# Kernel tuning notes

Measured on AMD Instinct MI355X. Metric: run time of the kernel, lower is better.

Reference implementation:

```python
import jax, jax.numpy as jnp
import numpy as np

B, N, D, K = 32, 2048, 512, 128
GAMMA = 10.0      # entropy_regularizer_weight
STEPS = 10        # optimization_steps
EPS = 1e-12


def _l2_normalize(x):
    return x * jax.lax.rsqrt(jnp.sum(x * x, axis=-1, keepdims=True) + EPS)


def setup_inputs() -> dict:
    key = jax.random.key(0)
    k1, k2, k3, k4 = jax.random.split(key, 4)
    features = jax.random.normal(k1, (B, N, D), dtype=jnp.float32)
    # transport ratio mu in (0,1): fraction of mass sent to the support
    transport_ratio = jax.random.uniform(k2, (B,), dtype=jnp.float32, minval=0.3, maxval=0.7)
    c_u = jax.random.uniform(k3, (B, N), dtype=jnp.float32)
    limit = float(np.sqrt(6.0 / (K + D)))  # GlorotUniform for (K, D) weight
    target_support = jax.random.uniform(k4, (K, D), dtype=jnp.float32, minval=-limit, maxval=limit)
    return {"features": features, "transport_ratio": transport_ratio,
            "c_u": c_u, "target_support": target_support}


def reference(features, transport_ratio, c_u, target_support):
    # --- binary costs: pairwise squared L2 between l2-normalized support and features ---
    f = _l2_normalize(features)          # [B, N, D]
    t = _l2_normalize(target_support)    # [K, D]
    cb = (jnp.sum(t * t, axis=-1)[None, :, None]
          + jnp.sum(f * f, axis=-1)[:, None, :]
          - 2.0 * jnp.einsum('kd,bnd->bkn', t, f))          # [B, K, N]
    C = jnp.concatenate([c_u[:, None, :], cb], axis=1)       # [B, K+1, N], row 0 = unary (discard) cost
    mu = transport_ratio[:, None, None]                      # [B, 1, 1]

    # --- entropy-regularized partial OT: Sinkhorn-style alternating scaling ---
    Q0 = jnp.exp(-GAMMA * C)
    n = jnp.asarray(C.shape[-1], C.dtype)

    def step(_, Q):
        # project onto column marginal: each feature carries mass 1/N
        Q = Q / (jnp.sum(Q, axis=1, keepdims=True) * n + EPS)
        # project onto row-mass constraints: support rows carry total mu, discard row 1-mu
        s0 = jnp.sum(Q[:, :1], axis=(1, 2), keepdims=True)
        ss = jnp.sum(Q[:, 1:], axis=(1, 2), keepdims=True)
        Q = jnp.concatenate([Q[:, :1] * (1.0 - mu) / (s0 + EPS),
                             Q[:, 1:] * mu / (ss + EPS)], axis=1)
        return Q

    Q = jax.lax.fori_loop(0, STEPS, step, Q0)
    # final column projection so each feature's transported mass is exactly 1/N
    P = Q / (jnp.sum(Q, axis=1, keepdims=True) * n + EPS)    # [B, K+1, N]
    return P
```

## Files before the change

### kernel.cpp

```cpp
#include <hip/hip_runtime.h>
#include <math.h>

#define B_ 32
#define N_ 2048
#define D_ 512
#define K_ 128
#define GAMMA_ 10.0f
#define EPS_ 1e-12f
#define STEPS_ 10
#define SHIFT_ 18.0f
#define EXP_NEG_SHIFT_ 1.5229979e-08f

typedef _Float16 f16x8 __attribute__((ext_vector_type(8)));
typedef _Float16 f16x4 __attribute__((ext_vector_type(4)));
typedef float f32x16 __attribute__((ext_vector_type(16)));

__global__ void k_prep_t(const float* __restrict__ ts, _Float16* __restrict__ tq,
                         float* __restrict__ rt, float* __restrict__ tnn) {
    int k = blockIdx.x;
    int lane = threadIdx.x;
    const float4* rp = (const float4*)(ts + (size_t)k * D_ + lane * 8);
    float4 v0 = rp[0], v1 = rp[1];
    f16x8 hv;
    hv[0] = (_Float16)v0.x; hv[1] = (_Float16)v0.y; hv[2] = (_Float16)v0.z; hv[3] = (_Float16)v0.w;
    hv[4] = (_Float16)v1.x; hv[5] = (_Float16)v1.y; hv[6] = (_Float16)v1.z; hv[7] = (_Float16)v1.w;
    float ssq = 0.f;
#pragma unroll
    for (int j = 0; j < 8; ++j) { float x = (float)hv[j]; ssq += x * x; }
#pragma unroll
    for (int off = 32; off; off >>= 1) ssq += __shfl_xor(ssq, off);
    if (lane == 0) {
        float rtv = (float)(1.0 / sqrt((double)ssq + 1e-12));
        rt[k] = rtv;
        tnn[k] = ssq * rtv * rtv;
    }
    *(f16x8*)&tq[((size_t)lane * 128 + k) * 8] = hv;
}

__global__ __launch_bounds__(256, 6) void k_gemm(
    const float* __restrict__ features,
    const _Float16* __restrict__ tq,
    const float* __restrict__ rt, const float* __restrict__ tnn,
    _Float16* __restrict__ E,
    float* __restrict__ A1)
{
    __shared__ _Float16 Bf[2][32 * 64];
    __shared__ float rowssq[32];
    __shared__ float csum[4][32];
    __shared__ float ldsrt[128], ldstnn[128];

    const int tid = threadIdx.x;
    const int b = blockIdx.x >> 6;
    const int n0 = (blockIdx.x & 63) * 32;
    const int w = tid >> 6;
    const int l = tid & 63;
    const int hi = l >> 5;
    const int l31 = l & 31;

    if (tid < 128) { ldsrt[tid] = rt[tid]; ldstnn[tid] = tnn[tid]; }

    const int fq = tid & 7;
    const int r0 = tid >> 3;
    const float4* fbase = (const float4*)(features + ((size_t)(b * N_ + n0)) * D_);

    float ss = 0.f;
    f32x16 acc;
#pragma unroll
    for (int i = 0; i < 16; ++i) acc[i] = 0.f;

    float4 br[2];
    f16x8 apre[4];

    auto stage_load = [&](int c) {
#pragma unroll
        for (int i = 0; i < 2; ++i)
            br[i] = fbase[(size_t)r0 * 128 + c * 16 + fq + i * 8];
    };

    auto a_load = [&](int c) {
#pragma unroll
        for (int ks = 0; ks < 4; ++ks) {
            int sB = ks * 2 + hi;
            size_t u = (size_t)(c * 8 + sB) * 128 + w * 32 + l31;
            apre[ks] = *(const f16x8*)&tq[u * 8];
        }
    };

    auto stage_write = [&](int buf) {
#pragma unroll
        for (int i = 0; i < 2; ++i) {
            float4 v = br[i];
            f16x4 hv;
            hv[0] = (_Float16)v.x; hv[1] = (_Float16)v.y;
            hv[2] = (_Float16)v.z; hv[3] = (_Float16)v.w;
            float q0 = (float)hv[0], q1 = (float)hv[1], q2 = (float)hv[2], q3 = (float)hv[3];
            ss += q0 * q0 + q1 * q1 + q2 * q2 + q3 * q3;
            int q = fq + i * 8;
            int s = q >> 1;
            int hh = q & 1;
            int idx = r0 * 64 + ((s ^ (r0 & 7)) << 3) + hh * 4;
            *(f16x4*)&Bf[buf][idx] = hv;
        }
    };

    auto compute = [&](int cur) {
#pragma unroll
        for (int ks = 0; ks < 4; ++ks) {
            int sB = ks * 2 + hi;
            f16x8 bfr = *(const f16x8*)&Bf[cur][l31 * 64 + ((sB ^ (l31 & 7)) << 3)];
            acc = __builtin_amdgcn_mfma_f32_32x32x16_f16(apre[ks], bfr, acc, 0, 0, 0);
        }
    };

    stage_load(0);
    a_load(0);
    stage_write(0);
    __syncthreads();

#pragma unroll
    for (int c = 0; c < 8; ++c) {
        int cur = c & 1;
        if (c < 7) stage_load(c + 1);
        compute(cur);
        if (c < 7) a_load(c + 1);
        if (c < 7) stage_write(cur ^ 1);
        __syncthreads();
    }

    ss += __shfl_xor(ss, 1);
    ss += __shfl_xor(ss, 2);
    ss += __shfl_xor(ss, 4);
    if (fq == 0) rowssq[r0] = ss;
    __syncthreads();

    const int n = n0 + l31;
    float rsq = rowssq[l31];
    float rf = (float)(1.0 / sqrt((double)rsq + 1e-12));
    float fnn = rsq * rf * rf;
    float cs = 0.f;
#pragma unroll
    for (int r = 0; r < 16; ++r) {
        int krow = (r & 3) + 8 * (r >> 2) + 4 * hi;
        int k = w * 32 + krow;
        float cb = ldstnn[k] + fnn - 2.0f * ldsrt[k] * rf * acc[r];
        float e = expf(SHIFT_ - GAMMA_ * cb);
        _Float16 eh = (_Float16)e;
        cs += (float)eh;
        E[((size_t)(b * K_ + k)) * N_ + n] = eh;
    }
    cs += __shfl_xor(cs, 32);
    if (!hi) csum[w][l31] = cs;
    __syncthreads();
    if (tid < 32)
        A1[b * N_ + n0 + tid] = csum[0][tid] + csum[1][tid] + csum[2][tid] + csum[3][tid];
}

__global__ __launch_bounds__(256) void k_sinkhorn(const float* __restrict__ tr,
                                                  const float* __restrict__ c_u,
                                                  const float* __restrict__ A1,
                                                  float* __restrict__ out,
                                                  float* __restrict__ wfb) {
    __shared__ float sc0[4], sc1[4], sres[2];
    int b = blockIdx.x, tid = threadIdx.x;
    float mu = tr[b];
    const float nf = (float)N_;
    float a0[8], a1[8], w[8];
#pragma unroll
    for (int r = 0; r < 8; ++r) {
        int n = tid + 256 * r;
        a0[r] = expf(-GAMMA_ * c_u[b * N_ + n]);
        a1[r] = A1[b * N_ + n] * EXP_NEG_SHIFT_;
        w[r] = 1.f;
    }
    float alpha = 1.f, beta = 1.f;
    for (int s = 0; s < STEPS_; ++s) {
        float p0 = 0.f, p1 = 0.f;
#pragma unroll
        for (int r = 0; r < 8; ++r) {
            float cs = w[r] * (alpha * a0[r] + beta * a1[r]);
            w[r] = w[r] / (cs * nf + EPS_);
            p0 += a0[r] * w[r];
            p1 += a1[r] * w[r];
        }
#pragma unroll
        for (int off = 32; off; off >>= 1) {
            p0 += __shfl_xor(p0, off);
            p1 += __shfl_xor(p1, off);
        }
        int wid = tid >> 6;
        if ((tid & 63) == 0) { sc0[wid] = p0; sc1[wid] = p1; }
        __syncthreads();
        if (tid == 0) {
            sres[0] = sc0[0] + sc0[1] + sc0[2] + sc0[3];
            sres[1] = sc1[0] + sc1[1] + sc1[2] + sc1[3];
        }
        __syncthreads();
        float s0 = alpha * sres[0], ssum = beta * sres[1];
        alpha *= (1.f - mu) / (s0 + EPS_);
        beta *= mu / (ssum + EPS_);
    }
#pragma unroll
    for (int r = 0; r < 8; ++r) {
        int n = tid + 256 * r;
        float cs = w[r] * (alpha * a0[r] + beta * a1[r]);
        float wf = w[r] / (cs * nf + EPS_);
        out[(size_t)b * (K_ + 1) * N_ + n] = alpha * a0[r] * wf;
        wfb[b * N_ + n] = beta * wf * EXP_NEG_SHIFT_;
    }
}

__global__ void k_scale(const _Float16* __restrict__ E, const float* __restrict__ wfb,
                        float* __restrict__ out) {
    size_t g = (size_t)blockIdx.x * 256 + threadIdx.x;
    size_t idx = g * 8;
    int b = (int)(idx >> 18);
    int rem = (int)(idx & ((K_ * N_) - 1));
    int k = rem >> 11, n = rem & (N_ - 1);
    f16x8 e = *(const f16x8*)&E[idx];
    float4 w0 = *(const float4*)&wfb[b * N_ + n];
    float4 w1 = *(const float4*)&wfb[b * N_ + n + 4];
    float* op = &out[((size_t)(b * (K_ + 1) + 1 + k)) * N_ + n];
    float4 o0, o1;
    o0.x = (float)e[0] * w0.x; o0.y = (float)e[1] * w0.y;
    o0.z = (float)e[2] * w0.z; o0.w = (float)e[3] * w0.w;
    o1.x = (float)e[4] * w1.x; o1.y = (float)e[5] * w1.y;
    o1.z = (float)e[6] * w1.z; o1.w = (float)e[7] * w1.w;
    *(float4*)op = o0;
    *(float4*)(op + 4) = o1;
}

extern "C" void kernel_launch(void* const* d_in, const int* in_sizes, int n_in,
                              void* d_out, int out_size, void* d_ws, size_t ws_size,
                              hipStream_t stream) {
    const float* features = (const float*)d_in[0];
    const float* tr = (const float*)d_in[1];
    const float* c_u = (const float*)d_in[2];
    const float* ts = (const float*)d_in[3];
    float* out = (float*)d_out;

    char* ws = (char*)d_ws;
    _Float16* tq = (_Float16*)ws;
    float* rt = (float*)(ws + 131072);
    float* tnn = (float*)(ws + 131584);
    float* A1 = (float*)(ws + 132096);
    float* wfb = (float*)(ws + 132096 + 262144);
    _Float16* E = (_Float16*)(ws + 132096 + 524288);
    (void)in_sizes; (void)n_in; (void)out_size; (void)ws_size;

    k_prep_t<<<K_, 64, 0, stream>>>(ts, tq, rt, tnn);
    k_gemm<<<B_ * 64, 256, 0, stream>>>(features, tq, rt, tnn, E, A1);
    k_sinkhorn<<<B_, 256, 0, stream>>>(tr, c_u, A1, out, wfb);
    k_scale<<<(B_ * K_ * N_) / (8 * 256), 256, 0, stream>>>(E, wfb, out);
}
```

Before: 54.63 us.

## Stage features into LDS via direct global-to-LDS loads as fp32

Features are now copied straight from global memory into an fp32 LDS double buffer with the async global_load_lds instruction, instead of going through registers, converting to fp16 and then storing. The fp16 conversion and the sum-of-squares row norm move into the MFMA compute loop, so each wave works out the row norms itself and the LDS reduction plus its extra barrier are gone. The aim is to cut register staging, VGPR pressure and store instructions. In exchange LDS use doubles, more conversion work sits on the critical compute path, and the norm is now computed from fp32 values rather than the fp16-rounded ones.

```diff
diff --git a/kernel.cpp b/kernel.cpp
--- a/kernel.cpp
+++ b/kernel.cpp
@@ -12,8 +12,13 @@
 #define EXP_NEG_SHIFT_ 1.5229979e-08f
 
 typedef _Float16 f16x8 __attribute__((ext_vector_type(8)));
-typedef _Float16 f16x4 __attribute__((ext_vector_type(4)));
+typedef float f32x8 __attribute__((ext_vector_type(8)));
 typedef float f32x16 __attribute__((ext_vector_type(16)));
+
+__device__ __forceinline__ void gload_lds16(const float4* g, float* l) {
+    __builtin_amdgcn_global_load_lds((const __attribute__((address_space(1))) void*)g,
+                                     (__attribute__((address_space(3))) void*)l, 16, 0, 0);
+}
 
 __global__ void k_prep_t(const float* __restrict__ ts, _Float16* __restrict__ tq,
                          float* __restrict__ rt, float* __restrict__ tnn) {
@@ -44,8 +49,7 @@
     _Float16* __restrict__ E,
     float* __restrict__ A1)
 {
-    __shared__ _Float16 Bf[2][32 * 64];
-    __shared__ float rowssq[32];
+    __shared__ float Bf32[2][32 * 64];
     __shared__ float csum[4][32];
     __shared__ float ldsrt[128], ldstnn[128];
 
@@ -59,22 +63,23 @@
 
     if (tid < 128) { ldsrt[tid] = rt[tid]; ldstnn[tid] = tnn[tid]; }
 
-    const int fq = tid & 7;
-    const int r0 = tid >> 3;
     const float4* fbase = (const float4*)(features + ((size_t)(b * N_ + n0)) * D_);
+
+    const int o0 = w * 128 + l;
+    const int r0s = o0 >> 4, q0s = (o0 & 15) ^ ((r0s & 7) << 1);
+    const int o1 = o0 + 64;
+    const int r1s = o1 >> 4, q1s = (o1 & 15) ^ ((r1s & 7) << 1);
 
     float ss = 0.f;
     f32x16 acc;
 #pragma unroll
     for (int i = 0; i < 16; ++i) acc[i] = 0.f;
 
-    float4 br[2];
     f16x8 apre[4];
 
-    auto stage_load = [&](int c) {
-#pragma unroll
-        for (int i = 0; i < 2; ++i)
-            br[i] = fbase[(size_t)r0 * 128 + c * 16 + fq + i * 8];
+    auto stage = [&](int c, int buf) {
+        gload_lds16(fbase + (size_t)r0s * 128 + c * 16 + q0s, &Bf32[buf][o0 * 4]);
+        gload_lds16(fbase + (size_t)r1s * 128 + c * 16 + q1s, &Bf32[buf][o1 * 4]);
     };
 
     auto a_load = [&](int c) {
@@ -86,57 +91,39 @@
         }
     };
 
-    auto stage_write = [&](int buf) {
-#pragma unroll
-        for (int i = 0; i < 2; ++i) {
-            float4 v = br[i];
-            f16x4 hv;
-            hv[0] = (_Float16)v.x; hv[1] = (_Float16)v.y;
-            hv[2] = (_Float16)v.z; hv[3] = (_Float16)v.w;
-            float q0 = (float)hv[0], q1 = (float)hv[1], q2 = (float)hv[2], q3 = (float)hv[3];
-            ss += q0 * q0 + q1 * q1 + q2 * q2 + q3 * q3;
-            int q = fq + i * 8;
-            int s = q >> 1;
-            int hh = q & 1;
-            int idx = r0 * 64 + ((s ^ (r0 & 7)) << 3) + hh * 4;
-            *(f16x4*)&Bf[buf][idx] = hv;
-        }
-    };
-
     auto compute = [&](int cur) {
 #pragma unroll
         for (int ks = 0; ks < 4; ++ks) {
             int sB = ks * 2 + hi;
-            f16x8 bfr = *(const f16x8*)&Bf[cur][l31 * 64 + ((sB ^ (l31 & 7)) << 3)];
+            int sp = sB ^ (l31 & 7);
+            f32x8 braw = *(const f32x8*)&Bf32[cur][l31 * 64 + sp * 8];
+            f16x8 bfr;
+#pragma unroll
+            for (int i = 0; i < 8; ++i) {
+                ss += braw[i] * braw[i];
+                bfr[i] = (_Float16)braw[i];
+            }
             acc = __builtin_amdgcn_mfma_f32_32x32x16_f16(apre[ks], bfr, acc, 0, 0, 0);
         }
     };
 
-    stage_load(0);
+    stage(0, 0);
     a_load(0);
-    stage_write(0);
     __syncthreads();
 
 #pragma unroll
     for (int c = 0; c < 8; ++c) {
         int cur = c & 1;
-        if (c < 7) stage_load(c + 1);
+        if (c < 7) stage(c + 1, cur ^ 1);
         compute(cur);
         if (c < 7) a_load(c + 1);
-        if (c < 7) stage_write(cur ^ 1);
         __syncthreads();
     }
 
-    ss += __shfl_xor(ss, 1);
-    ss += __shfl_xor(ss, 2);
-    ss += __shfl_xor(ss, 4);
-    if (fq == 0) rowssq[r0] = ss;
-    __syncthreads();
-
+    ss += __shfl_xor(ss, 32);
     const int n = n0 + l31;
-    float rsq = rowssq[l31];
-    float rf = (float)(1.0 / sqrt((double)rsq + 1e-12));
-    float fnn = rsq * rf * rf;
+    float rf = (float)(1.0 / sqrt((double)ss + 1e-12));
+    float fnn = ss * rf * rf;
     float cs = 0.f;
 #pragma unroll
     for (int r = 0; r < 16; ++r) {
```

New measurement: 58.32 us. 1.07x slower.
